# Kernel tuning notes

Hardware: AMD Instinct MI355X
Metric: run time of the kernel (lower is better)

The kernel has to match this reference:

```python
import jax, jax.numpy as jnp
import numpy as np

EMBED_DIM = 1024
BATCH = 4
SEQ = 2048


def setup_inputs() -> dict:
    key = jax.random.key(0)
    ks = jax.random.split(key, 9)
    D = EMBED_DIM
    s = 1.0 / np.sqrt(D)
    inputs = jax.random.normal(ks[0], (BATCH, SEQ, D), dtype=jnp.float32)
    rotation_params = jax.random.normal(ks[1], (D, D), dtype=jnp.float32) * s
    entangle_params = jax.random.normal(ks[2], (D, D), dtype=jnp.float32) * s
    Wq = jax.random.normal(ks[3], (D, D), dtype=jnp.float32) * s
    bq = jax.random.normal(ks[4], (D,), dtype=jnp.float32) * 0.01
    Wk = jax.random.normal(ks[5], (D, D), dtype=jnp.float32) * s
    bk = jax.random.normal(ks[6], (D,), dtype=jnp.float32) * 0.01
    Wv = jax.random.normal(ks[7], (D, D), dtype=jnp.float32) * s
    bv = jax.random.normal(ks[8], (D,), dtype=jnp.float32) * 0.01
    # causal mask: True = masked out (matches torch masked_fill semantics)
    mask = jnp.triu(jnp.ones((SEQ, SEQ), dtype=bool), k=1)
    return {"inputs": inputs, "rotation_params": rotation_params,
            "entangle_params": entangle_params, "Wq": Wq, "bq": bq,
            "Wk": Wk, "bk": bk, "Wv": Wv, "bv": bv, "mask": mask}


def reference(inputs, rotation_params, entangle_params, Wq, bq, Wk, bk, Wv, bv, mask):
    D = inputs.shape[-1]
    # q = Linear(x) @ R^T ; k = Linear(x) @ E^T ; v = Linear(x)
    q = (jnp.einsum('bsd,ed->bse', inputs, Wq) + bq) @ rotation_params.T
    k = (jnp.einsum('bsd,ed->bse', inputs, Wk) + bk) @ entangle_params.T
    v = jnp.einsum('bsd,ed->bse', inputs, Wv) + bv
    scores = jnp.einsum('bqd,bkd->bqk', q, k) / jnp.sqrt(jnp.float32(D))
    scores = jnp.where(mask, jnp.float32(-jnp.inf), scores)
    probs = jax.nn.softmax(scores, axis=-1)  # dropout=0.0 -> identity
    return jnp.einsum('bqk,bkd->bqd', probs, v)
```

## Files before the change

### kernel.cpp

```cpp
#include <hip/hip_runtime.h>
#include <hip/hip_bf16.h>
#include <stdint.h>
#include <math.h>

#define DD 1024
#define SS 2048
#define BB 4

typedef __bf16 bf16;
typedef __bf16 bf16x8 __attribute__((ext_vector_type(8)));
typedef __bf16 bf16x4 __attribute__((ext_vector_type(4)));
typedef float f32x4 __attribute__((ext_vector_type(4)));

__device__ __forceinline__ void gload_lds16(const bf16* g, bf16* l) {
  __builtin_amdgcn_global_load_lds(
      (const __attribute__((address_space(1))) void*)g,
      (__attribute__((address_space(3))) void*)l, 16, 0, 0);
}

__global__ __launch_bounds__(256) void prep_all(
    const float* __restrict__ x, const float* __restrict__ R,
    const float* __restrict__ E, const float* __restrict__ Wv,
    const float* __restrict__ Wq, const float* __restrict__ Wk,
    const float* __restrict__ bq, const float* __restrict__ bk,
    const float* __restrict__ bv, bf16* __restrict__ xb,
    bf16* __restrict__ Rb, bf16* __restrict__ Eb, bf16* __restrict__ Wvb,
    bf16* __restrict__ WqT, bf16* __restrict__ WkT, float* __restrict__ bias,
    float* __restrict__ rowsums) {
  int bid = blockIdx.x;
  int t = threadIdx.x;
  if (bid < 11264) {
    const float* src;
    bf16* dst;
    int base;
    if (bid < 8192) { src = x; dst = xb; base = bid; }
    else if (bid < 9216) { src = R; dst = Rb; base = bid - 8192; }
    else if (bid < 10240) { src = E; dst = Eb; base = bid - 9216; }
    else { src = Wv; dst = Wvb; base = bid - 10240; }
    int i = (base * 256 + t) * 4;
    float4 v = *(const float4*)(src + i);
    bf16x4 o;
    o.x = (bf16)v.x; o.y = (bf16)v.y; o.z = (bf16)v.z; o.w = (bf16)v.w;
    *(bf16x4*)(dst + i) = o;
  } else if (bid < 13312) {
    int r2 = bid - 11264;
    const float* src = (r2 >= 1024) ? Wk : Wq;
    bf16* dst = (r2 >= 1024) ? WkT : WqT;
    int rem = r2 & 1023;
    int bx = rem & 31, by = rem >> 5;
    __shared__ float tile[32][33];
    int tx = t & 31, ty = t >> 5;
    int xcol = bx * 32 + tx;
    int y0 = by * 32;
    for (int r = ty; r < 32; r += 8)
      tile[r][tx] = src[(y0 + r) * DD + xcol];
    __syncthreads();
    int dx = by * 32 + tx;
    int dy0 = bx * 32;
    for (int r = ty; r < 32; r += 8)
      dst[(dy0 + r) * DD + dx] = (bf16)tile[tx][r];
  } else if (bid < 16384) {
    int e = bid - 13312;
    if (e >= 2048) { if (t == 0) bias[e] = bv[e - 2048]; return; }
    const float* M = (e < 1024) ? R : E;
    const float* bb = (e < 1024) ? bq : bk;
    int row = e & 1023;
    float s = 0.f;
    for (int f = t; f < DD; f += 256) s += M[row * DD + f] * bb[f];
    for (int o = 32; o >= 1; o >>= 1) s += __shfl_xor(s, o, 64);
    __shared__ float red[4];
    if ((t & 63) == 0) red[t >> 6] = s;
    __syncthreads();
    if (t == 0) bias[e] = red[0] + red[1] + red[2] + red[3];
  } else {
    int idx = (bid - 16384) * 256 + t;
    rowsums[idx] = 0.f;
  }
}

template <int MODE>
__global__ __launch_bounds__(256, 4)
void gemm_bt(const bf16* __restrict__ Ag, long lda, long sAb,
             const bf16* __restrict__ Bg, long ldb, long sBb,
             void* __restrict__ Cg, long ldc, long sCb,
             const float* __restrict__ bias, float scale, int K,
             bf16* __restrict__ vTp, float* __restrict__ rowsums) {
  __shared__ __align__(16) bf16 smem[16384];
  bf16* As = smem;
  bf16* Bs = smem + 8192;

  int bx = blockIdx.x, by = blockIdx.y, bz = blockIdx.z;
  if (MODE == 1) {
    int q = bx;
    by = (int)((sqrtf(8.f * q + 1.f) - 1.f) * 0.5f);
    while ((by + 1) * (by + 2) / 2 <= q) by++;
    while (by * (by + 1) / 2 > q) by--;
    bx = q - by * (by + 1) / 2;
  }
  if (MODE == 2) by = 15 - by;
  long m0 = (long)by * 128, n0 = (long)bx * 128;
  const bf16* A = Ag + (long)bz * sAb + m0 * lda;
  const bf16* Bp = Bg + (long)bz * sBb + n0 * ldb;

  int t = threadIdx.x;
  int w = t >> 6, l = t & 63;
  int lr = l >> 2;
  int lc = (((l & 3) ^ (lr & 3)) * 8);
  int quad = l >> 4, ln = l & 15;
  int wm = w >> 1, wn = w & 1;
  int rdoff = ((quad ^ (ln & 3)) * 8);

  int Keff = (MODE == 2) ? (by + 1) * 128 : K;

  f32x4 acc[4][4];
#pragma unroll
  for (int i = 0; i < 4; i++)
#pragma unroll
    for (int j = 0; j < 4; j++) acc[i][j] = f32x4{0.f, 0.f, 0.f, 0.f};

  const bf16* a_base = As + (wm * 64 + ln) * 32 + rdoff;
  const bf16* b_base = Bs + (wn * 64 + ln) * 32 + rdoff;
  long arow0 = (long)(w * 16 + lr);

  for (int k0 = 0; k0 < Keff; k0 += 64) {
#pragma unroll
    for (int kk = 0; kk < 2; kk++) {
      int kc = k0 + kk * 32 + lc;
      gload_lds16(A + arow0 * lda + kc, As + kk * 4096 + w * 512);
      gload_lds16(A + (arow0 + 64) * lda + kc, As + kk * 4096 + 2048 + w * 512);
      gload_lds16(Bp + arow0 * ldb + kc, Bs + kk * 4096 + w * 512);
      gload_lds16(Bp + (arow0 + 64) * ldb + kc, Bs + kk * 4096 + 2048 + w * 512);
    }
    asm volatile("s_waitcnt vmcnt(0)" ::: "memory");
    __syncthreads();

#pragma unroll
    for (int kk = 0; kk < 2; kk++) {
      bf16x8 af[4], bfr[4];
#pragma unroll
      for (int i = 0; i < 4; i++) {
        af[i] = *(const bf16x8*)(a_base + kk * 4096 + i * 512);
        bfr[i] = *(const bf16x8*)(b_base + kk * 4096 + i * 512);
      }
#pragma unroll
      for (int i = 0; i < 4; i++)
#pragma unroll
        for (int j = 0; j < 4; j++)
          acc[i][j] = __builtin_amdgcn_mfma_f32_16x16x32_bf16(
              af[i], bfr[j], acc[i][j], 0, 0, 0);
    }
    __syncthreads();
  }

  if (MODE == 0) {
    if (vTp && n0 >= 2048) {
      int d0 = (int)n0 - 2048;
      int b = (int)(m0 >> 11);
      int s0 = (int)(m0 & 2047);
#pragma unroll
      for (int i = 0; i < 4; i++) {
        int sb = wm * 64 + i * 16 + quad * 4;
#pragma unroll
        for (int j = 0; j < 4; j++) {
          int d = wn * 64 + j * 16 + ln;
          float bv_ = bias[n0 + d];
#pragma unroll
          for (int r = 0; r < 4; r++)
            smem[d * 128 + ((sb + r) ^ (ln << 3))] = (bf16)(acc[i][j][r] + bv_);
        }
      }
      __syncthreads();
      int d = t >> 1, h = t & 1;
      bf16* dst = vTp + (long)b * DD * SS + (long)(d0 + d) * SS + s0 + h * 64;
#pragma unroll
      for (int j = 0; j < 8; j++) {
        int sbase = h * 64 + j * 8;
        bf16x8 v = *(const bf16x8*)(smem + d * 128 + (sbase ^ ((d & 15) << 3)));
        *(bf16x8*)(dst + j * 8) = v;
      }
    } else {
      bf16* C = (bf16*)Cg + (long)bz * sCb + m0 * ldc + n0;
#pragma unroll
      for (int i = 0; i < 4; i++) {
        int rb = wm * 64 + i * 16 + quad * 4;
#pragma unroll
        for (int j = 0; j < 4; j++) {
          int col = wn * 64 + j * 16 + ln;
          float bv_ = bias ? bias[n0 + col] : 0.f;
#pragma unroll
          for (int r = 0; r < 4; r++)
            C[(long)(rb + r) * ldc + col] = (bf16)(acc[i][j][r] + bv_);
        }
      }
    }
  } else if (MODE == 1) {
#pragma unroll
    for (int i = 0; i < 4; i++) {
      int rb = wm * 64 + i * 16 + quad * 4;
#pragma unroll
      for (int j = 0; j < 4; j++) {
        int col = wn * 64 + j * 16 + ln;
#pragma unroll
        for (int r = 0; r < 4; r++) {
          int row = rb + r;
          float p = 0.f;
          if (n0 + col <= m0 + row) p = __expf(acc[i][j][r] * scale);
          smem[row * 128 + (col ^ ((row & 15) << 3))] = (bf16)p;
        }
      }
    }
    __syncthreads();
    int row = t >> 1, h = t & 1;
    bf16* P = (bf16*)Cg + (long)bz * sCb + (m0 + row) * ldc + n0;
    float rsum = 0.f;
#pragma unroll
    for (int jj = 0; jj < 8; jj++) {
      int p8 = h * 8 + jj;
      int slot = p8 ^ (row & 15);
      bf16x8 v = *(const bf16x8*)(smem + row * 128 + slot * 8);
#pragma unroll
      for (int e = 0; e < 8; e++) rsum += (float)v[e];
      *(bf16x8*)(P + p8 * 8) = v;
    }
    atomicAdd(&rowsums[(long)bz * SS + m0 + row], rsum);
  } else {
    float* C = (float*)Cg + (long)bz * sCb + m0 * ldc + n0;
    const float* rs = rowsums + (long)bz * SS + m0;
#pragma unroll
    for (int i = 0; i < 4; i++) {
      int rb = wm * 64 + i * 16 + quad * 4;
      float inv[4];
#pragma unroll
      for (int r = 0; r < 4; r++) inv[r] = 1.f / rs[rb + r];
#pragma unroll
      for (int j = 0; j < 4; j++) {
        int col = wn * 64 + j * 16 + ln;
#pragma unroll
        for (int r = 0; r < 4; r++)
          C[(long)(rb + r) * ldc + col] = acc[i][j][r] * inv[r];
      }
    }
  }
}

extern "C" void kernel_launch(void* const* d_in, const int* in_sizes, int n_in,
                              void* d_out, int out_size, void* d_ws,
                              size_t ws_size, hipStream_t stream) {
  const float* x = (const float*)d_in[0];
  const float* R = (const float*)d_in[1];
  const float* E = (const float*)d_in[2];
  const float* Wq = (const float*)d_in[3];
  const float* bq = (const float*)d_in[4];
  const float* Wk = (const float*)d_in[5];
  const float* bk = (const float*)d_in[6];
  const float* Wv = (const float*)d_in[7];
  const float* bv = (const float*)d_in[8];
  float* out = (float*)d_out;

  char* ws = (char*)d_ws;
  bf16* qkv = (bf16*)ws;
  bf16* vT = (bf16*)(ws + 50331648);
  bf16* probs = (bf16*)(ws + 67108864);
  float* rowsums = (float*)(ws + 100663296);
  char* sr = ws + 101711872;
  bf16* xb = (bf16*)sr;
  bf16* Rb = (bf16*)(sr + 16777216);
  bf16* Eb = Rb + 1024 * 1024;
  bf16* WqT = (bf16*)(sr + 20971520);
  bf16* WkT = WqT + 1024 * 1024;
  bf16* wcat = (bf16*)(sr + 25165824);
  float* bias = (float*)(sr + 31457280);

  prep_all<<<16416, 256, 0, stream>>>(x, R, E, Wv, Wq, Wk, bq, bk, bv, xb, Rb,
                                      Eb, wcat + 2048 * DD, WqT, WkT, bias,
                                      rowsums);

  gemm_bt<0><<<dim3(8, 8, 2), 256, 0, stream>>>(
      Rb, DD, 1024 * 1024, WqT, DD, 1024 * 1024, wcat, DD, 1024 * 1024,
      nullptr, 1.f, DD, nullptr, nullptr);

  gemm_bt<0><<<dim3(24, 64, 1), 256, 0, stream>>>(xb, DD, 0, wcat, DD, 0, qkv,
                                                  3072, 0, bias, 1.f, DD, vT,
                                                  nullptr);

  gemm_bt<1><<<dim3(136, 1, BB), 256, 0, stream>>>(
      qkv, 3072, (long)SS * 3072, qkv + 1024, 3072, (long)SS * 3072, probs,
      SS, (long)SS * SS, nullptr, 0.03125f, DD, nullptr, rowsums);

  gemm_bt<2><<<dim3(8, 16, BB), 256, 0, stream>>>(
      probs, SS, (long)SS * SS, vT, SS, (long)DD * SS, out,
      DD, (long)SS * DD, nullptr, 1.f, SS, nullptr, rowsums);
}
```

Before: 303.0 us.

## Fold Q and K projections into a single D×D bilinear form on x

Rewrites the scores as x·M·xᵀ plus a per-key bias term, where M = Wqᵀ·Rᵀ·E·Wk is precomputed by small weight-only GEMMs. Softmax is invariant to the per-query constant, so bk is dropped. The big projection GEMM now produces only T = x·M and V (2048 output columns instead of 3072), and the QK GEMM multiplies T by x directly. A small GEMV fused into the GEMM launches computes the per-key bias beta = x·(Wkᵀ·Eᵀ·R·bq). This adds three chained 1024³ GEMMs and changes rounding, because bf16 is applied to the combined matrix and to x instead of to q and k.

```diff
diff --git a/kernel.cpp b/kernel.cpp
--- a/kernel.cpp
+++ b/kernel.cpp
@@ -20,33 +20,30 @@
 
 __global__ __launch_bounds__(256) void prep_all(
     const float* __restrict__ x, const float* __restrict__ R,
-    const float* __restrict__ E, const float* __restrict__ Wv,
-    const float* __restrict__ Wq, const float* __restrict__ Wk,
-    const float* __restrict__ bq, const float* __restrict__ bk,
-    const float* __restrict__ bv, bf16* __restrict__ xb,
-    bf16* __restrict__ Rb, bf16* __restrict__ Eb, bf16* __restrict__ Wvb,
-    bf16* __restrict__ WqT, bf16* __restrict__ WkT, float* __restrict__ bias,
+    const float* __restrict__ E, const float* __restrict__ Wq,
+    const float* __restrict__ Wk, const float* __restrict__ Wv,
+    bf16* __restrict__ xb, bf16* __restrict__ RT, bf16* __restrict__ ET,
+    bf16* __restrict__ WqT, bf16* __restrict__ WkT, bf16* __restrict__ wcat,
     float* __restrict__ rowsums) {
   int bid = blockIdx.x;
   int t = threadIdx.x;
-  if (bid < 11264) {
+  if (bid < 9216) {
     const float* src;
     bf16* dst;
     int base;
     if (bid < 8192) { src = x; dst = xb; base = bid; }
-    else if (bid < 9216) { src = R; dst = Rb; base = bid - 8192; }
-    else if (bid < 10240) { src = E; dst = Eb; base = bid - 9216; }
-    else { src = Wv; dst = Wvb; base = bid - 10240; }
+    else { src = Wv; dst = wcat + 1024 * 1024; base = bid - 8192; }
     int i = (base * 256 + t) * 4;
     float4 v = *(const float4*)(src + i);
     bf16x4 o;
     o.x = (bf16)v.x; o.y = (bf16)v.y; o.z = (bf16)v.z; o.w = (bf16)v.w;
     *(bf16x4*)(dst + i) = o;
   } else if (bid < 13312) {
-    int r2 = bid - 11264;
-    const float* src = (r2 >= 1024) ? Wk : Wq;
-    bf16* dst = (r2 >= 1024) ? WkT : WqT;
-    int rem = r2 & 1023;
+    int idx = bid - 9216;
+    int which = idx >> 10;
+    const float* src = (which == 0) ? R : (which == 1) ? E : (which == 2) ? Wq : Wk;
+    bf16* dst = (which == 0) ? RT : (which == 1) ? ET : (which == 2) ? WqT : WkT;
+    int rem = idx & 1023;
     int bx = rem & 31, by = rem >> 5;
     __shared__ float tile[32][33];
     int tx = t & 31, ty = t >> 5;
@@ -59,21 +56,8 @@
     int dy0 = bx * 32;
     for (int r = ty; r < 32; r += 8)
       dst[(dy0 + r) * DD + dx] = (bf16)tile[tx][r];
-  } else if (bid < 16384) {
-    int e = bid - 13312;
-    if (e >= 2048) { if (t == 0) bias[e] = bv[e - 2048]; return; }
-    const float* M = (e < 1024) ? R : E;
-    const float* bb = (e < 1024) ? bq : bk;
-    int row = e & 1023;
-    float s = 0.f;
-    for (int f = t; f < DD; f += 256) s += M[row * DD + f] * bb[f];
-    for (int o = 32; o >= 1; o >>= 1) s += __shfl_xor(s, o, 64);
-    __shared__ float red[4];
-    if ((t & 63) == 0) red[t >> 6] = s;
-    __syncthreads();
-    if (t == 0) bias[e] = red[0] + red[1] + red[2] + red[3];
   } else {
-    int idx = (bid - 16384) * 256 + t;
+    int idx = (bid - 13312) * 256 + t;
     rowsums[idx] = 0.f;
   }
 }
@@ -84,12 +68,32 @@
              const bf16* __restrict__ Bg, long ldb, long sBb,
              void* __restrict__ Cg, long ldc, long sCb,
              const float* __restrict__ bias, float scale, int K,
-             bf16* __restrict__ vTp, float* __restrict__ rowsums) {
+             bf16* __restrict__ vTp, float* __restrict__ rowsums,
+             const bf16* __restrict__ gA, const float* __restrict__ gx,
+             float* __restrict__ gy, int gemvBx) {
   __shared__ __align__(16) bf16 smem[16384];
   bf16* As = smem;
   bf16* Bs = smem + 8192;
 
   int bx = blockIdx.x, by = blockIdx.y, bz = blockIdx.z;
+  int t = threadIdx.x;
+
+  if ((MODE == 0 || MODE == 4) && gy && bx == gemvBx) {
+    int r = t >> 1, h = t & 1;
+    long row = (long)by * 128 + r;
+    const bf16* ap = gA + row * 1024 + h * 512;
+    const float* xp = gx + h * 512;
+    float s = 0.f;
+    for (int k = 0; k < 512; k += 8) {
+      bf16x8 a8 = *(const bf16x8*)(ap + k);
+#pragma unroll
+      for (int e = 0; e < 8; e++) s += (float)a8[e] * xp[k + e];
+    }
+    s += __shfl_xor(s, 1, 64);
+    if (h == 0) gy[row] = s;
+    return;
+  }
+
   if (MODE == 1) {
     int q = bx;
     by = (int)((sqrtf(8.f * q + 1.f) - 1.f) * 0.5f);
@@ -102,7 +106,6 @@
   const bf16* A = Ag + (long)bz * sAb + m0 * lda;
   const bf16* Bp = Bg + (long)bz * sBb + n0 * ldb;
 
-  int t = threadIdx.x;
   int w = t >> 6, l = t & 63;
   int lr = l >> 2;
   int lc = (((l & 3) ^ (lr & 3)) * 8);
@@ -152,59 +155,76 @@
     __syncthreads();
   }
 
-  if (MODE == 0) {
-    if (vTp && n0 >= 2048) {
-      int d0 = (int)n0 - 2048;
-      int b = (int)(m0 >> 11);
-      int s0 = (int)(m0 & 2047);
-#pragma unroll
-      for (int i = 0; i < 4; i++) {
-        int sb = wm * 64 + i * 16 + quad * 4;
-#pragma unroll
-        for (int j = 0; j < 4; j++) {
-          int d = wn * 64 + j * 16 + ln;
-          float bv_ = bias[n0 + d];
-#pragma unroll
-          for (int r = 0; r < 4; r++)
-            smem[d * 128 + ((sb + r) ^ (ln << 3))] = (bf16)(acc[i][j][r] + bv_);
-        }
-      }
-      __syncthreads();
-      int d = t >> 1, h = t & 1;
-      bf16* dst = vTp + (long)b * DD * SS + (long)(d0 + d) * SS + s0 + h * 64;
-#pragma unroll
-      for (int j = 0; j < 8; j++) {
-        int sbase = h * 64 + j * 8;
-        bf16x8 v = *(const bf16x8*)(smem + d * 128 + (sbase ^ ((d & 15) << 3)));
-        *(bf16x8*)(dst + j * 8) = v;
-      }
-    } else {
-      bf16* C = (bf16*)Cg + (long)bz * sCb + m0 * ldc + n0;
-#pragma unroll
-      for (int i = 0; i < 4; i++) {
-        int rb = wm * 64 + i * 16 + quad * 4;
-#pragma unroll
-        for (int j = 0; j < 4; j++) {
-          int col = wn * 64 + j * 16 + ln;
-          float bv_ = bias ? bias[n0 + col] : 0.f;
-#pragma unroll
-          for (int r = 0; r < 4; r++)
-            C[(long)(rb + r) * ldc + col] = (bf16)(acc[i][j][r] + bv_);
-        }
-      }
-    }
-  } else if (MODE == 1) {
+  bool transposed = (MODE == 3) || (MODE == 4 && n0 >= 1024);
+  if ((MODE == 0 || MODE == 4) && !transposed) {
+    bf16* C = (bf16*)Cg + (long)bz * sCb + m0 * ldc + n0;
+    const float* bptr = (MODE == 4) ? nullptr : bias;
 #pragma unroll
     for (int i = 0; i < 4; i++) {
       int rb = wm * 64 + i * 16 + quad * 4;
 #pragma unroll
       for (int j = 0; j < 4; j++) {
         int col = wn * 64 + j * 16 + ln;
+        float bv_ = bptr ? bptr[n0 + col] : 0.f;
+#pragma unroll
+        for (int r = 0; r < 4; r++)
+          C[(long)(rb + r) * ldc + col] = (bf16)(acc[i][j][r] + bv_);
+      }
+    }
+  } else if (transposed) {
+    bf16* tb;
+    long tld;
+    int d0i, s0i;
+    const float* bptr;
+    if (MODE == 4) {
+      tb = vTp + (m0 >> 11) * (long)DD * SS;
+      tld = SS;
+      d0i = (int)n0 - 1024;
+      s0i = (int)(m0 & 2047);
+      bptr = bias;
+    } else {
+      tb = (bf16*)Cg;
+      tld = ldc;
+      d0i = (int)n0;
+      s0i = (int)m0;
+      bptr = nullptr;
+    }
+#pragma unroll
+    for (int i = 0; i < 4; i++) {
+      int sb = wm * 64 + i * 16 + quad * 4;
+#pragma unroll
+      for (int j = 0; j < 4; j++) {
+        int d = wn * 64 + j * 16 + ln;
+        float bv_ = bptr ? bptr[d0i + d] : 0.f;
+#pragma unroll
+        for (int r = 0; r < 4; r++)
+          smem[d * 128 + ((sb + r) ^ (ln << 3))] = (bf16)(acc[i][j][r] + bv_);
+      }
+    }
+    __syncthreads();
+    int d = t >> 1, h = t & 1;
+    bf16* dst = tb + (long)(d0i + d) * tld + s0i + h * 64;
+#pragma unroll
+    for (int j = 0; j < 8; j++) {
+      int sbase = h * 64 + j * 8;
+      bf16x8 v = *(const bf16x8*)(smem + d * 128 + (sbase ^ ((d & 15) << 3)));
+      *(bf16x8*)(dst + j * 8) = v;
+    }
+  } else if (MODE == 1) {
+    const float* betap = bias + (long)bz * SS + n0;
+#pragma unroll
+    for (int i = 0; i < 4; i++) {
+      int rb = wm * 64 + i * 16 + quad * 4;
+#pragma unroll
+      for (int j = 0; j < 4; j++) {
+        int col = wn * 64 + j * 16 + ln;
+        float bcol = betap[col];
 #pragma unroll
         for (int r = 0; r < 4; r++) {
           int row = rb + r;
           float p = 0.f;
-          if (n0 + col <= m0 + row) p = __expf(acc[i][j][r] * scale);
+          if (n0 + col <= m0 + row)
+            p = __expf((acc[i][j][r] + bcol) * scale);
           smem[row * 128 + (col ^ ((row & 15) << 3))] = (bf16)p;
         }
       }
@@ -252,42 +272,48 @@
   const float* Wq = (const float*)d_in[3];
   const float* bq = (const float*)d_in[4];
   const float* Wk = (const float*)d_in[5];
-  const float* bk = (const float*)d_in[6];
   const float* Wv = (const float*)d_in[7];
   const float* bv = (const float*)d_in[8];
   float* out = (float*)d_out;
 
   char* ws = (char*)d_ws;
-  bf16* qkv = (bf16*)ws;
-  bf16* vT = (bf16*)(ws + 50331648);
-  bf16* probs = (bf16*)(ws + 67108864);
+  bf16* xb = (bf16*)ws;
+  bf16* Tbuf = (bf16*)(ws + 16777216);
+  bf16* vT = (bf16*)(ws + 33554432);
+  bf16* probs = (bf16*)(ws + 50331648);
+  bf16* RT = (bf16*)(ws + 83886080);
+  bf16* ET = (bf16*)(ws + 85983232);
+  bf16* WqT = (bf16*)(ws + 88080384);
+  bf16* WkT = (bf16*)(ws + 90177536);
+  bf16* GpT = (bf16*)(ws + 92274688);
+  bf16* Hb = (bf16*)(ws + 94371840);
+  bf16* wcat = (bf16*)(ws + 96468992);
   float* rowsums = (float*)(ws + 100663296);
-  char* sr = ws + 101711872;
-  bf16* xb = (bf16*)sr;
-  bf16* Rb = (bf16*)(sr + 16777216);
-  bf16* Eb = Rb + 1024 * 1024;
-  bf16* WqT = (bf16*)(sr + 20971520);
-  bf16* WkT = WqT + 1024 * 1024;
-  bf16* wcat = (bf16*)(sr + 25165824);
-  float* bias = (float*)(sr + 31457280);
-
-  prep_all<<<16416, 256, 0, stream>>>(x, R, E, Wv, Wq, Wk, bq, bk, bv, xb, Rb,
-                                      Eb, wcat + 2048 * DD, WqT, WkT, bias,
-                                      rowsums);
-
-  gemm_bt<0><<<dim3(8, 8, 2), 256, 0, stream>>>(
-      Rb, DD, 1024 * 1024, WqT, DD, 1024 * 1024, wcat, DD, 1024 * 1024,
-      nullptr, 1.f, DD, nullptr, nullptr);
-
-  gemm_bt<0><<<dim3(24, 64, 1), 256, 0, stream>>>(xb, DD, 0, wcat, DD, 0, qkv,
-                                                  3072, 0, bias, 1.f, DD, vT,
-                                                  nullptr);
+  float* beta = (float*)(ws + 100696064);
+  float* vvec = (float*)(ws + 100728832);
+
+  prep_all<<<13344, 256, 0, stream>>>(x, R, E, Wq, Wk, Wv, xb, RT, ET, WqT,
+                                      WkT, wcat, rowsums);
+
+  gemm_bt<3><<<dim3(8, 8, 1), 256, 0, stream>>>(
+      ET, DD, 0, RT, DD, 0, GpT, DD, 0, nullptr, 1.f, DD, nullptr, nullptr,
+      nullptr, nullptr, nullptr, -1);
+  gemm_bt<0><<<dim3(8, 8, 1), 256, 0, stream>>>(
+      WkT, DD, 0, GpT, DD, 0, Hb, DD, 0, nullptr, 1.f, DD, nullptr, nullptr,
+      nullptr, nullptr, nullptr, -1);
+  gemm_bt<0><<<dim3(9, 8, 1), 256, 0, stream>>>(
+      Hb, DD, 0, WqT, DD, 0, wcat, DD, 0, nullptr, 1.f, DD, nullptr, nullptr,
+      Hb, bq, vvec, 8);
+
+  gemm_bt<4><<<dim3(17, 64, 1), 256, 0, stream>>>(
+      xb, DD, 0, wcat, DD, 0, Tbuf, DD, 0, bv, 1.f, DD, vT, nullptr, xb, vvec,
+      beta, 16);
 
   gemm_bt<1><<<dim3(136, 1, BB), 256, 0, stream>>>(
-      qkv, 3072, (long)SS * 3072, qkv + 1024, 3072, (long)SS * 3072, probs,
-      SS, (long)SS * SS, nullptr, 0.03125f, DD, nullptr, rowsums);
+      Tbuf, DD, (long)SS * DD, xb, DD, (long)SS * DD, probs, SS, (long)SS * SS,
+      beta, 0.03125f, DD, nullptr, rowsums, nullptr, nullptr, nullptr, -1);
 
   gemm_bt<2><<<dim3(8, 16, BB), 256, 0, stream>>>(
-      probs, SS, (long)SS * SS, vT, SS, (long)DD * SS, out,
-      DD, (long)SS * DD, nullptr, 1.f, SS, nullptr, rowsums);
+      probs, SS, (long)SS * SS, vT, SS, (long)DD * SS, out, DD, (long)SS * DD,
+      nullptr, 1.f, SS, nullptr, rowsums, nullptr, nullptr, nullptr, -1);
 }
```

After: 337.0 us. +11.2%, slower.
